# Kernel optimization log

Hardware: AMD Instinct MI355X
Metric: run time of the kernel (lower is better)

The kernel has to match this reference:

```python
import jax, jax.numpy as jnp
import numpy as np

B, T, C, H = 16, 4096, 256, 256

def setup_inputs() -> dict:
    key = jax.random.key(0)
    kx, kwi, kbi, kwh, kbh = jax.random.split(key, 5)
    s = 1.0 / np.sqrt(C)
    return {
        "x": jax.random.normal(kx, (B, T, C), dtype=jnp.float32),
        "Wi": jax.random.uniform(kwi, (H, C), dtype=jnp.float32, minval=-s, maxval=s),
        "bi": jax.random.uniform(kbi, (H,), dtype=jnp.float32, minval=-s, maxval=s),
        "Wh": jax.random.uniform(kwh, (H, H), dtype=jnp.float32, minval=-s, maxval=s),
        "bh": jax.random.uniform(kbh, (H,), dtype=jnp.float32, minval=-s, maxval=s),
    }

def reference(x, Wi, bi, Wh, bh):
    # Faithful to the source: Cell computes tanh(i2h(x) + h2h(x)) -- both
    # linears applied to x_t, the hidden state is never consumed, so there
    # is no recurrence and all timesteps can be computed in one fused pass.
    # hidden_states: [B, T, H]
    hidden_states = jnp.tanh(
        jnp.einsum("btc,hc->bth", x, Wi) + bi
        + jnp.einsum("btc,hc->bth", x, Wh) + bh
    )
    h_last = hidden_states[:, -1, :]  # h after the loop
    return (hidden_states, h_last)
```

## Files before the change

### kernel.cpp

```cpp
#include <hip/hip_runtime.h>


using short8 = __attribute__((ext_vector_type(8))) short;
using f32x4  = __attribute__((ext_vector_type(4))) float;

constexpr int Tn = 4096, Cn = 256, Hn = 256;
constexpr int Mn = 16 * Tn;

__device__ inline unsigned pack2_bf16(float a, float b) {
  unsigned ua = __float_as_uint(a);
  unsigned ub = __float_as_uint(b);
  ua += 0x7fffu + ((ua >> 16) & 1u);
  ub += 0x7fffu + ((ub >> 16) & 1u);
  return (ua >> 16) | (ub & 0xffff0000u);
}

union u4s8 { uint4 u; short8 s; };

__global__ __launch_bounds__(256) void prep_kernel(
    const float* __restrict__ Wi, const float* __restrict__ bi,
    const float* __restrict__ Wh, const float* __restrict__ bh,
    unsigned short* __restrict__ Wc, float* __restrict__ bc) {
  int idx = blockIdx.x * 256 + threadIdx.x;
  float w = Wi[idx] + Wh[idx];
  unsigned u = __float_as_uint(w);
  u += 0x7fffu + ((u >> 16) & 1u);
  Wc[idx] = (unsigned short)(u >> 16);
  if (blockIdx.x == 0) bc[threadIdx.x] = bi[threadIdx.x] + bh[threadIdx.x];
}

__global__ __launch_bounds__(512, 4) void gemm_tanh_kernel(
    const float* __restrict__ x, const unsigned short* __restrict__ Wc,
    const float* __restrict__ bc, float* __restrict__ out) {
  __shared__ __align__(16) unsigned short Bsm[128 * 256];

  const int tid   = threadIdx.x;
  const int bid   = blockIdx.x;
  const int mb    = bid & 511;
  const int nb    = bid >> 9;
  const int mBase = mb * 128;
  const int nBase = nb * 128;

  const int wave = tid >> 6;
  const int lane = tid & 63;
  const int rid  = lane & 15;
  const int kgrp = lane >> 4;
  const int rowBase = mBase + wave * 16;

  uint4 wbuf[8];
  int wr[8], wc[8];
#pragma unroll
  for (int i = 0; i < 8; i++) {
    int h = i * 512 + tid;
    wr[i] = h >> 5;
    wc[i] = h & 31;
    wbuf[i] = *(const uint4*)(Wc + (size_t)(nBase + wr[i]) * Cn + wc[i] * 8);
  }

  const float* ap = x + (size_t)(rowBase + rid) * Cn + kgrp * 8;
  float4 abuf[8][2];
#pragma unroll
  for (int kc = 0; kc < 8; kc++) {
    const float4* p = (const float4*)(ap + kc * 32);
    abuf[kc][0] = p[0];
    abuf[kc][1] = p[1];
  }

  __builtin_amdgcn_sched_barrier(0);

#pragma unroll
  for (int i = 0; i < 8; i++) {
    int pc = wc[i] ^ (wr[i] & 7);
    *(uint4*)&Bsm[(wr[i] << 8) + (pc << 3)] = wbuf[i];
  }
  __syncthreads();

  f32x4 acc[8];
#pragma unroll
  for (int in = 0; in < 8; in++) acc[in] = (f32x4)0.f;

#pragma unroll
  for (int kc = 0; kc < 8; kc++) {
    u4s8 t0;
    t0.u.x = pack2_bf16(abuf[kc][0].x, abuf[kc][0].y);
    t0.u.y = pack2_bf16(abuf[kc][0].z, abuf[kc][0].w);
    t0.u.z = pack2_bf16(abuf[kc][1].x, abuf[kc][1].y);
    t0.u.w = pack2_bf16(abuf[kc][1].z, abuf[kc][1].w);
    short8 af = t0.s;

    const int cbase = (kc << 2) | kgrp;
#pragma unroll
    for (int in = 0; in < 8; in++) {
      int ln = in * 16 + rid;
      short8 bf = *(const short8*)&Bsm[(ln << 8) + ((cbase ^ (ln & 7)) << 3)];
      acc[in] = __builtin_amdgcn_mfma_f32_16x16x32_bf16(af, bf, acc[in], 0, 0, 0);
    }
  }

#pragma unroll
  for (int in = 0; in < 8; in++) {
    int n = nBase + in * 16 + rid;
    float bias = bc[n];
    int mrow = rowBase + kgrp * 4;
#pragma unroll
    for (int r = 0; r < 4; r++) {
      int m = mrow + r;
      float v = acc[in][r] + bias;
      float t = 1.f - 2.f / (__expf(2.f * v) + 1.f);
      out[(size_t)m * Hn + n] = t;
      if ((m & (Tn - 1)) == (Tn - 1))
        out[(size_t)Mn * Hn + (size_t)(m >> 12) * Hn + n] = t;
    }
  }
}

extern "C" void kernel_launch(void* const* d_in, const int* in_sizes, int n_in,
                              void* d_out, int out_size, void* d_ws,
                              size_t ws_size, hipStream_t stream) {
  (void)in_sizes; (void)n_in; (void)out_size; (void)ws_size;
  const float* x  = (const float*)d_in[0];
  const float* Wi = (const float*)d_in[1];
  const float* bi = (const float*)d_in[2];
  const float* Wh = (const float*)d_in[3];
  const float* bh = (const float*)d_in[4];
  float* out = (float*)d_out;

  unsigned short* Wc = (unsigned short*)d_ws;
  float* bc = (float*)((char*)d_ws + (size_t)Hn * Cn * sizeof(unsigned short));

  prep_kernel<<<(Hn * Cn) / 256, 256, 0, stream>>>(Wi, bi, Wh, bh, Wc, bc);
  gemm_tanh_kernel<<<1024, 512, 0, stream>>>(x, Wc, bc, out);
}
```

Before: 145.3 us.

## Give each block full N width with register-held weights and double-buffered LDS x streaming

Each block now covers 256 rows across all 256 output columns. This lets x be read from global memory once instead of once per N-half. The combined bf16 weights are kept in registers per wave, and fp32 x tiles of 64 rows are streamed into double-buffered LDS with global_load_lds, using an XOR swizzle for conflict-free reads. The grid drops to 256 blocks of 1024 threads with 128KB of LDS each, which trades occupancy and launch parallelism for less global traffic and overlap of loads with MFMA work.

New measurement: 144.8 us. About the same (-0.4%).

```diff
diff --git a/kernel.cpp b/kernel.cpp
--- a/kernel.cpp
+++ b/kernel.cpp
@@ -6,6 +6,9 @@
 
 constexpr int Tn = 4096, Cn = 256, Hn = 256;
 constexpr int Mn = 16 * Tn;
+constexpr int STEP = 64;
+constexpr int RPB  = 256;
+constexpr int NSTEPS = RPB / STEP;
 
 __device__ inline unsigned pack2_bf16(float a, float b) {
   unsigned ua = __float_as_uint(a);
@@ -14,8 +17,6 @@
   ub += 0x7fffu + ((ub >> 16) & 1u);
   return (ua >> 16) | (ub & 0xffff0000u);
 }
-
-union u4s8 { uint4 u; short8 s; };
 
 __global__ __launch_bounds__(256) void prep_kernel(
     const float* __restrict__ Wi, const float* __restrict__ bi,
@@ -29,88 +30,102 @@
   if (blockIdx.x == 0) bc[threadIdx.x] = bi[threadIdx.x] + bh[threadIdx.x];
 }
 
-__global__ __launch_bounds__(512, 4) void gemm_tanh_kernel(
+__global__ __launch_bounds__(1024, 4) void gemm_tanh_kernel(
     const float* __restrict__ x, const unsigned short* __restrict__ Wc,
     const float* __restrict__ bc, float* __restrict__ out) {
-  __shared__ __align__(16) unsigned short Bsm[128 * 256];
+  __shared__ __align__(16) float Abuf[2][STEP * Cn];
 
-  const int tid   = threadIdx.x;
-  const int bid   = blockIdx.x;
-  const int mb    = bid & 511;
-  const int nb    = bid >> 9;
-  const int mBase = mb * 128;
-  const int nBase = nb * 128;
-
+  const int tid  = threadIdx.x;
   const int wave = tid >> 6;
   const int lane = tid & 63;
   const int rid  = lane & 15;
   const int kgrp = lane >> 4;
-  const int rowBase = mBase + wave * 16;
+  const int wy   = wave >> 3;
+  const int wx   = wave & 7;
+  const int mBase = blockIdx.x * RPB;
 
-  uint4 wbuf[8];
-  int wr[8], wc[8];
+  auto issue = [&](int s, int b) {
+    const float* src = x + (size_t)(mBase + s * STEP) * Cn;
 #pragma unroll
-  for (int i = 0; i < 8; i++) {
-    int h = i * 512 + tid;
-    wr[i] = h >> 5;
-    wc[i] = h & 31;
-    wbuf[i] = *(const uint4*)(Wc + (size_t)(nBase + wr[i]) * Cn + wc[i] * 8);
-  }
+    for (int rr = 0; rr < 4; rr++) {
+      int r = wave * 4 + rr;
+      int c = lane ^ (r & 7);
+      const float* g = src + r * Cn + c * 4;
+      __builtin_amdgcn_global_load_lds(
+          (const __attribute__((address_space(1))) unsigned int*)g,
+          (__attribute__((address_space(3))) unsigned int*)&Abuf[b][r * Cn],
+          16, 0, 0);
+    }
+  };
 
-  const float* ap = x + (size_t)(rowBase + rid) * Cn + kgrp * 8;
-  float4 abuf[8][2];
+  issue(0, 0);
+
+  short8 bf[2][8];
+  float  bias[2];
 #pragma unroll
-  for (int kc = 0; kc < 8; kc++) {
-    const float4* p = (const float4*)(ap + kc * 32);
-    abuf[kc][0] = p[0];
-    abuf[kc][1] = p[1];
-  }
-
-  __builtin_amdgcn_sched_barrier(0);
-
+  for (int jn = 0; jn < 2; jn++) {
+    int n = wx * 32 + jn * 16 + rid;
+    bias[jn] = bc[n];
 #pragma unroll
-  for (int i = 0; i < 8; i++) {
-    int pc = wc[i] ^ (wr[i] & 7);
-    *(uint4*)&Bsm[(wr[i] << 8) + (pc << 3)] = wbuf[i];
+    for (int kc = 0; kc < 8; kc++)
+      bf[jn][kc] = *(const short8*)&Wc[(size_t)n * Cn + kc * 32 + kgrp * 8];
   }
   __syncthreads();
 
-  f32x4 acc[8];
+  for (int s = 0; s < NSTEPS; s++) {
+    const int b = s & 1;
+    if (s + 1 < NSTEPS) issue(s + 1, b ^ 1);
+    __builtin_amdgcn_sched_barrier(0);
+
+    f32x4 acc[2][2];
 #pragma unroll
-  for (int in = 0; in < 8; in++) acc[in] = (f32x4)0.f;
+    for (int im = 0; im < 2; im++)
+#pragma unroll
+      for (int jn = 0; jn < 2; jn++) acc[im][jn] = (f32x4)0.f;
+
+    const float* base = &Abuf[b][0];
+#pragma unroll
+    for (int kc = 0; kc < 8; kc++) {
+      short8 af[2];
+#pragma unroll
+      for (int im = 0; im < 2; im++) {
+        int lr = wy * 32 + im * 16 + rid;
+        int c0 = kc * 8 + kgrp * 2;
+        float4 v0 = *(const float4*)&base[lr * Cn + ((c0 ^ (lr & 7)) << 2)];
+        float4 v1 = *(const float4*)&base[lr * Cn + (((c0 + 1) ^ (lr & 7)) << 2)];
+        union { uint4 u; short8 s; } t;
+        t.u.x = pack2_bf16(v0.x, v0.y);
+        t.u.y = pack2_bf16(v0.z, v0.w);
+        t.u.z = pack2_bf16(v1.x, v1.y);
+        t.u.w = pack2_bf16(v1.z, v1.w);
+        af[im] = t.s;
+      }
+#pragma unroll
+      for (int im = 0; im < 2; im++)
+#pragma unroll
+        for (int jn = 0; jn < 2; jn++)
+          acc[im][jn] = __builtin_amdgcn_mfma_f32_16x16x32_bf16(
+              af[im], bf[jn][kc], acc[im][jn], 0, 0, 0);
+    }
 
 #pragma unroll
-  for (int kc = 0; kc < 8; kc++) {
-    u4s8 t0;
-    t0.u.x = pack2_bf16(abuf[kc][0].x, abuf[kc][0].y);
-    t0.u.y = pack2_bf16(abuf[kc][0].z, abuf[kc][0].w);
-    t0.u.z = pack2_bf16(abuf[kc][1].x, abuf[kc][1].y);
-    t0.u.w = pack2_bf16(abuf[kc][1].z, abuf[kc][1].w);
-    short8 af = t0.s;
+    for (int im = 0; im < 2; im++)
+#pragma unroll
+      for (int jn = 0; jn < 2; jn++) {
+        int n  = wx * 32 + jn * 16 + rid;
+        int m0 = mBase + s * STEP + wy * 32 + im * 16 + kgrp * 4;
+#pragma unroll
+        for (int r = 0; r < 4; r++) {
+          int m = m0 + r;
+          float v = acc[im][jn][r] + bias[jn];
+          float t = 1.f - 2.f / (__expf(2.f * v) + 1.f);
+          out[(size_t)m * Hn + n] = t;
+          if ((m & (Tn - 1)) == (Tn - 1))
+            out[(size_t)Mn * Hn + (size_t)(m >> 12) * Hn + n] = t;
+        }
+      }
 
-    const int cbase = (kc << 2) | kgrp;
-#pragma unroll
-    for (int in = 0; in < 8; in++) {
-      int ln = in * 16 + rid;
-      short8 bf = *(const short8*)&Bsm[(ln << 8) + ((cbase ^ (ln & 7)) << 3)];
-      acc[in] = __builtin_amdgcn_mfma_f32_16x16x32_bf16(af, bf, acc[in], 0, 0, 0);
-    }
-  }
-
-#pragma unroll
-  for (int in = 0; in < 8; in++) {
-    int n = nBase + in * 16 + rid;
-    float bias = bc[n];
-    int mrow = rowBase + kgrp * 4;
-#pragma unroll
-    for (int r = 0; r < 4; r++) {
-      int m = mrow + r;
-      float v = acc[in][r] + bias;
-      float t = 1.f - 2.f / (__expf(2.f * v) + 1.f);
-      out[(size_t)m * Hn + n] = t;
-      if ((m & (Tn - 1)) == (Tn - 1))
-        out[(size_t)Mn * Hn + (size_t)(m >> 12) * Hn + n] = t;
-    }
+    __syncthreads();
   }
 }
 
@@ -129,5 +144,5 @@
   float* bc = (float*)((char*)d_ws + (size_t)Hn * Cn * sizeof(unsigned short));
 
   prep_kernel<<<(Hn * Cn) / 256, 256, 0, stream>>>(Wi, bi, Wh, bh, Wc, bc);
-  gemm_tanh_kernel<<<1024, 512, 0, stream>>>(x, Wc, bc, out);
+  gemm_tanh_kernel<<<256, 1024, 0, stream>>>(x, Wc, bc, out);
 }
```
